# Kernel optimization log

Hardware: AMD Instinct MI355X
Metric: run time of the kernel (lower is better)

Reference implementation:

```python
import jax, jax.numpy as jnp
import numpy as np

H = 64      # h_dim
E = 64      # embedding_dim
L = 100     # latent_dim
T = 30      # seq_len
DT = 0.03

def _leaky(x):
    return jnp.where(x >= 0, x, 0.01 * x)  # nn.LeakyReLU default slope

def _mlp(h, Ws, bs, Wf, bf):
    # 3 stacked [H,H] LeakyReLU layers + final [L,H] layer, LeakyReLU after EVERY layer (as in source)
    for i in range(Ws.shape[0]):
        h = _leaky(h @ Ws[i].T + bs[i])
    return _leaky(h @ Wf.T + bf)

def _lstm_step(h, c, gates):
    # torch LSTM gate order: i, f, g, o
    i, f, g, o = jnp.split(gates, 4, axis=-1)
    c = jax.nn.sigmoid(f) * c + jax.nn.sigmoid(i) * jnp.tanh(g)
    h = jax.nn.sigmoid(o) * jnp.tanh(c)
    return h, c

def _forward(expert_traj, init_state, eps,
             W_se, b_se,
             W_ih_e, W_hh_e, b_ih_e, b_hh_e,
             mean_Ws, mean_bs, mean_Wf, mean_bf,
             lv_Ws, lv_bs, lv_Wf, lv_bf,
             W_init, b_init,
             W_ih_d, W_hh_d, b_ih_d, b_hh_d,
             W_c, b_c):
    B = expert_traj.shape[0]
    # --- encode: relative positions ---
    rel_xy = jnp.concatenate([expert_traj[:, :1, :2],
                              expert_traj[:, 1:, :2] - expert_traj[:, :-1, :2]], axis=1)
    inp = jnp.concatenate([rel_xy, expert_traj[:, :, 2:]], axis=-1)  # [B,T,4]
    emb = inp @ W_se.T + b_se                                        # [B,T,E]
    x_seq = jnp.swapaxes(emb, 0, 1)                                  # [T,B,E] seq-major
    # precompute input projection for all timesteps in one GEMM
    xp = x_seq @ W_ih_e.T + (b_ih_e + b_hh_e)                        # [T,B,4H]
    h0 = jnp.zeros((B, H), dtype=expert_traj.dtype)
    c0 = jnp.zeros((B, H), dtype=expert_traj.dtype)
    def enc_step(carry, xp_t):
        h, c = carry
        h, c = _lstm_step(h, c, xp_t + h @ W_hh_e.T)
        return (h, c), None
    (hT, _), _ = jax.lax.scan(enc_step, (h0, c0), xp)
    mu = _mlp(hT, mean_Ws, mean_bs, mean_Wf, mean_bf)                # [B,L]
    log_var = _mlp(hT, lv_Ws, lv_bs, lv_Wf, lv_bf)                   # [B,L]
    # --- reparameterize + tanh ---
    z = jnp.tanh(eps * jnp.exp(0.5 * log_var) + mu)
    # --- decode ---
    dh = z @ W_init.T + b_init                                       # [B,H], h0 = c0 = dh
    bias_d = b_ih_d + b_hh_d
    def dec_step(carry, _):
        h, c, prev = carry
        xe = prev @ W_se.T + b_se                                    # spatial embedding of state
        h, c = _lstm_step(h, c, xe @ W_ih_d.T + h @ W_hh_d.T + bias_d)
        ctrl = h @ W_c.T + b_c                                       # [B,2]
        pedal = ctrl[:, 0]
        steer = jnp.clip(ctrl[:, 1], -0.5, 0.5)
        x_t, y_t, psi, v = prev[:, 0], prev[:, 1], prev[:, 2], prev[:, 3]
        v1 = jnp.clip(v + pedal * DT, 0.0, 30.0)
        psi_dot = jnp.clip(v * jnp.tan(steer) / 2.5, -3.14 / 2, 3.14 / 2)
        cur = jnp.stack([x_t + v * jnp.cos(psi) * DT,
                         y_t + v * jnp.sin(psi) * DT,
                         psi + psi_dot * DT,
                         v1], axis=1)
        return (h, c, cur), cur
    _, traj = jax.lax.scan(dec_step, (dh, dh, init_state), None, length=T)
    recons = jnp.swapaxes(traj, 0, 1)                                # [B,T,4]
    return recons, expert_traj, mu, log_var

def setup_inputs() -> dict:
    key = jax.random.key(0)
    ks = jax.random.split(key, 32)
    B = 16384
    s = 0.05
    def p(k, shape):
        return jax.random.normal(k, shape, dtype=jnp.float32) * s
    return {
        "expert_traj": jax.random.normal(ks[0], (B, T, 4), dtype=jnp.float32),
        "init_state": jax.random.normal(ks[1], (B, 4), dtype=jnp.float32),
        "eps": jax.random.normal(ks[2], (B, L), dtype=jnp.float32),
        "W_se": p(ks[3], (E, 4)), "b_se": p(ks[4], (E,)),
        "W_ih_e": p(ks[5], (4 * H, E)), "W_hh_e": p(ks[6], (4 * H, H)),
        "b_ih_e": p(ks[7], (4 * H,)), "b_hh_e": p(ks[8], (4 * H,)),
        "mean_Ws": p(ks[9], (3, H, H)), "mean_bs": p(ks[10], (3, H)),
        "mean_Wf": p(ks[11], (L, H)), "mean_bf": p(ks[12], (L,)),
        "lv_Ws": p(ks[13], (3, H, H)), "lv_bs": p(ks[14], (3, H)),
        "lv_Wf": p(ks[15], (L, H)), "lv_bf": p(ks[16], (L,)),
        "W_init": p(ks[17], (H, L)), "b_init": p(ks[18], (H,)),
        "W_ih_d": p(ks[19], (4 * H, E)), "W_hh_d": p(ks[20], (4 * H, H)),
        "b_ih_d": p(ks[21], (4 * H,)), "b_hh_d": p(ks[22], (4 * H,)),
        "W_c": p(ks[23], (2, H)), "b_c": p(ks[24], (2,)),
    }

def reference(expert_traj, init_state, eps,
              W_se, b_se,
              W_ih_e, W_hh_e, b_ih_e, b_hh_e,
              mean_Ws, mean_bs, mean_Wf, mean_bf,
              lv_Ws, lv_bs, lv_Wf, lv_bf,
              W_init, b_init,
              W_ih_d, W_hh_d, b_ih_d, b_hh_d,
              W_c, b_c):
    return _forward(expert_traj, init_state, eps,
                    W_se, b_se,
                    W_ih_e, W_hh_e, b_ih_e, b_hh_e,
                    mean_Ws, mean_bs, mean_Wf, mean_bf,
                    lv_Ws, lv_bs, lv_Wf, lv_bf,
                    W_init, b_init,
                    W_ih_d, W_hh_d, b_ih_d, b_hh_d,
                    W_c, b_c)
```

## Files before the change

kernel.cpp:

```cpp
#include <hip/hip_runtime.h>

typedef unsigned short u16;
typedef unsigned int u32;
typedef __attribute__((ext_vector_type(8))) short bf16x8;
typedef __attribute__((ext_vector_type(4))) float f32x4;

#define B_TOT 16384
#define RPW 16
#define BLK 64
#define NBLK (B_TOT / RPW)
#define TT 30
#define LL 100
#define DTC 0.03f
#define L2E 1.44269504088896f

#define HST 104

#define OFF_HS  0
#define OFF_XS  3328
#define OFF_INP 5376
#define OFF_ZB  9216
#define SMEM_SZ 13568

#define WS_WHHE  0
#define WS_WHHD  18432
#define WS_MWS   36864
#define WS_LWS   49152
#define WS_MWF   61440
#define WS_LWF   67840
#define WS_WINIT 74240
#define WS_TOTAL 82432

__device__ __forceinline__ float bf2f(u16 u) {
    union { u32 i; float f; } v; v.i = ((u32)u) << 16; return v.f;
}
__device__ __forceinline__ u16 f2bf(float f) {
    union { float f; u32 i; } v; v.f = f;
    return (u16)((v.i + 0x7FFFu + ((v.i >> 16) & 1u)) >> 16);
}
__device__ __forceinline__ u16 f2bf_t(float f) {
    union { float f; u32 i; } v; v.f = f;
    return (u16)(v.i >> 16);
}
__device__ __forceinline__ float rcpf(float x) { return __builtin_amdgcn_rcpf(x); }
__device__ __forceinline__ float ex2(float x) { return __builtin_amdgcn_exp2f(x); }
__device__ __forceinline__ float tanh_(float x) {
    x = fminf(fmaxf(x, -15.f), 15.f);
    float e = __expf(2.f * x);
    return (e - 1.f) * rcpf(e + 1.f);
}
__device__ __forceinline__ float leaky(float x) { return x >= 0.f ? x : 0.01f * x; }
__device__ __forceinline__ f32x4 mfma16(bf16x8 a, bf16x8 b, f32x4 c) {
    return __builtin_amdgcn_mfma_f32_16x16x32_bf16(a, b, c, 0, 0, 0);
}

__global__ void setup_kernel(
    const float* __restrict__ W_se, const float* __restrict__ b_se,
    const float* __restrict__ W_ih_e, const float* __restrict__ W_hh_e,
    const float* __restrict__ b_ih_e, const float* __restrict__ b_hh_e,
    const float* __restrict__ W_ih_d, const float* __restrict__ W_hh_d,
    const float* __restrict__ b_ih_d, const float* __restrict__ b_hh_d,
    const float* __restrict__ mean_Ws, const float* __restrict__ lv_Ws,
    const float* __restrict__ mean_Wf, const float* __restrict__ lv_Wf,
    const float* __restrict__ W_init, u16* __restrict__ ws)
{
    const int gid = blockIdx.x * 256 + threadIdx.x;
    const int nth = gridDim.x * 256;
    for (int i = gid; i < 512; i += nth) {
        int which = i >> 8, row = i & 255, g = row >> 6;
        float s = (g == 2) ? 2.f * L2E : L2E;
        const float* wih = (which ? W_ih_d : W_ih_e) + row * 64;
        float f0=0,f1=0,f2=0,f3=0,fb=0;
        for (int e = 0; e < 64; ++e) {
            float w = wih[e];
            f0 = fmaf(w, W_se[e*4+0], f0);
            f1 = fmaf(w, W_se[e*4+1], f1);
            f2 = fmaf(w, W_se[e*4+2], f2);
            f3 = fmaf(w, W_se[e*4+3], f3);
            fb = fmaf(w, b_se[e], fb);
        }
        fb += (which ? b_ih_d : b_ih_e)[row] + (which ? b_hh_d : b_hh_e)[row];
        u16* dst = ws + (which ? WS_WHHD : WS_WHHE) + row * 72 + 64;
        dst[0]=f2bf(f0*s); dst[1]=f2bf(f1*s); dst[2]=f2bf(f2*s); dst[3]=f2bf(f3*s);
        dst[4]=f2bf(fb*s); dst[5]=0; dst[6]=0; dst[7]=0;
    }
    for (int i = gid; i < 2*16384; i += nth) {
        int which = i >= 16384;
        int j = which ? i - 16384 : i;
        int row = j >> 6, k = j & 63, g = row >> 6;
        float s = (g == 2) ? 2.f * L2E : L2E;
        const float* whh = which ? W_hh_d : W_hh_e;
        ws[(which ? WS_WHHD : WS_WHHE) + row*72 + k] = f2bf(whh[j] * s);
    }
    for (int i = gid; i < 12288; i += nth) {
        ws[WS_MWS + i] = f2bf(mean_Ws[i]);
        ws[WS_LWS + i] = f2bf(lv_Ws[i]);
    }
    for (int i = gid; i < 6400; i += nth) {
        ws[WS_MWF + i] = f2bf(mean_Wf[i]);
        ws[WS_LWF + i] = f2bf(lv_Wf[i]);
    }
    for (int i = gid; i < 8192; i += nth) {
        int r = i >> 7, k = i & 127;
        ws[WS_WINIT + i] = (k < LL) ? f2bf(W_init[r*LL + k]) : (u16)0;
    }
}

__global__ __launch_bounds__(BLK, 1) void vae_lstm_kernel(
    const float* __restrict__ expert, const float* __restrict__ init_state,
    const float* __restrict__ eps, const u16* __restrict__ ws,
    const float* __restrict__ mean_bs, const float* __restrict__ mean_bf,
    const float* __restrict__ lv_bs, const float* __restrict__ lv_bf,
    const float* __restrict__ b_init, const float* __restrict__ W_c,
    const float* __restrict__ b_c,
    float* __restrict__ out_recons, float* __restrict__ out_expert,
    float* __restrict__ out_mu, float* __restrict__ out_lv)
{
    const int l = threadIdx.x;
    const int lcol = l & 15;
    const int quad = l >> 4;
    const int b0 = blockIdx.x * RPW;

    __shared__ __align__(16) char smem[SMEM_SZ];
    u16* Hs  = (u16*)(smem + OFF_HS);
    u16* XS  = (u16*)(smem + OFF_XS);
    u16* inp = (u16*)(smem + OFF_INP);
    u16* zB  = (u16*)(smem + OFF_ZB);

    {
        u32* hz = (u32*)Hs;
#pragma unroll
        for (int i = 0; i < 13; ++i) hz[l + i * 64] = 0;
        if (l < RPW) Hs[l*HST + 68] = 0x3F80;
        u32* zz = (u32*)zB;
#pragma unroll
        for (int i = 0; i < 17; ++i) zz[l + i * 64] = 0;
        const int base = b0 * (TT*4);
#pragma unroll 4
        for (int i = 0; i < 30; ++i) {
            int idx = l + i * 64;
            int row = idx / 120, q = idx % 120;
            int t = q >> 2, k = q & 3;
            float v = expert[base + idx];
            out_expert[base + idx] = v;
            float r = v;
            if (k < 2 && t > 0) r = v - expert[base + idx - 4];
            u16 hv = f2bf(r);
            inp[row*120 + q] = hv;
            if (t == 0) Hs[row*HST + 64 + k] = hv;
        }
        __syncthreads();
    }

    float cst[4][4] = {};
    float hval[4][4];
    bf16x8 bw[4][4][3];

    auto build_bw = [&](const u16* wsW) {
#pragma unroll
        for (int g = 0; g < 4; ++g)
#pragma unroll
            for (int u = 0; u < 4; ++u) {
                const u16* wr = wsW + (g*64 + u*16 + lcol) * 72;
                bw[g][u][0] = *(const bf16x8*)(wr + quad*8);
                bw[g][u][1] = *(const bf16x8*)(wr + 32 + quad*8);
                if (quad == 0) {
                    bw[g][u][2] = *(const bf16x8*)(wr + 64);
                } else {
                    bf16x8 z;
#pragma unroll
                    for (int j = 0; j < 8; ++j) z[j] = 0;
                    bw[g][u][2] = z;
                }
            }
    };

    auto lstm_step = [&]() {
        const u16* hrow = Hs + lcol*HST;
        bf16x8 a0 = *(const bf16x8*)(hrow + quad*8);
        bf16x8 a1 = *(const bf16x8*)(hrow + 32 + quad*8);
        bf16x8 a2 = *(const bf16x8*)(hrow + 64 + quad*8);
        f32x4 acc[4][4];
#pragma unroll
        for (int g = 0; g < 4; ++g)
#pragma unroll
            for (int u = 0; u < 4; ++u) {
                f32x4 z = {0.f, 0.f, 0.f, 0.f};
                z = mfma16(a0, bw[g][u][0], z);
                z = mfma16(a1, bw[g][u][1], z);
                acc[g][u] = mfma16(a2, bw[g][u][2], z);
            }
#pragma unroll
        for (int u = 0; u < 4; ++u)
#pragma unroll
            for (int r = 0; r < 4; ++r) {
                float Ei = ex2(-acc[0][u][r]);
                float Ef = ex2(-acc[1][u][r]);
                float Eg = ex2(-acc[2][u][r]);
                float Eo = ex2(-acc[3][u][r]);
                float P = (1.f + Ei) * (1.f + Eg);
                float Q = 1.f + Ef;
                float num = fmaf(cst[u][r], P, (1.f - Eg) * Q);
                float cc = num * rcpf(P * Q);
                cst[u][r] = cc;
                float Ec = ex2(-2.f * L2E * cc);
                float h = (1.f - Ec) * rcpf((1.f + Eo) * (1.f + Ec));
                hval[u][r] = h;
                Hs[(quad*4 + r)*HST + u*16 + lcol] = f2bf_t(h);
            }
    };

    build_bw(ws + WS_WHHE);
    for (int stp = 0; stp < TT; ++stp) {
        lstm_step();
        if (stp < TT - 1) {
            int row = l >> 2, k = l & 3;
            Hs[row*HST + 64 + k] = inp[row*120 + (stp + 1)*4 + k];
        }
    }

    auto mlp_hidden = [&](bf16x8 a0, bf16x8 a1, const u16* wsW, const float* bg,
                          u16* outB, int ost) {
#pragma unroll
        for (int u = 0; u < 4; ++u) {
            int n = u*16 + lcol;
            const u16* wr = wsW + n*64;
            bf16x8 bb0 = *(const bf16x8*)(wr + quad*8);
            bf16x8 bb1 = *(const bf16x8*)(wr + 32 + quad*8);
            float bv = bg[n];
            f32x4 acc = {bv, bv, bv, bv};
            acc = mfma16(a0, bb0, acc);
            acc = mfma16(a1, bb1, acc);
#pragma unroll
            for (int r = 0; r < 4; ++r)
                outB[(quad*4 + r)*ost + n] = f2bf_t(leaky(acc[r]));
        }
    };

    {
        bf16x8 t0 = *(const bf16x8*)(Hs + lcol*HST + quad*8);
        bf16x8 t1 = *(const bf16x8*)(Hs + lcol*HST + 32 + quad*8);
        mlp_hidden(t0, t1, ws + WS_MWS, mean_bs, XS, 64);
        mlp_hidden(t0, t1, ws + WS_LWS, lv_bs, Hs, HST);
        bf16x8 m0 = *(const bf16x8*)(XS + lcol*64 + quad*8);
        bf16x8 m1 = *(const bf16x8*)(XS + lcol*64 + 32 + quad*8);
        mlp_hidden(m0, m1, ws + WS_MWS + 4096, mean_bs + 64, XS, 64);
        bf16x8 v0 = *(const bf16x8*)(Hs + lcol*HST + quad*8);
        bf16x8 v1 = *(const bf16x8*)(Hs + lcol*HST + 32 + quad*8);
        mlp_hidden(v0, v1, ws + WS_LWS + 4096, lv_bs + 64, Hs, HST);
        m0 = *(const bf16x8*)(XS + lcol*64 + quad*8);
        m1 = *(const bf16x8*)(XS + lcol*64 + 32 + quad*8);
        mlp_hidden(m0, m1, ws + WS_MWS + 8192, mean_bs + 128, XS, 64);
        v0 = *(const bf16x8*)(Hs + lcol*HST + quad*8);
        v1 = *(const bf16x8*)(Hs + lcol*HST + 32 + quad*8);
        mlp_hidden(v0, v1, ws + WS_LWS + 8192, lv_bs + 128, Hs, HST);
    }

    float muv[7][4];

    {
        bf16x8 fa = *(const bf16x8*)(XS + lcol*64 + quad*8);
        bf16x8 fb = *(const bf16x8*)(XS + lcol*64 + 32 + quad*8);
#pragma unroll
        for (int nt = 0; nt < 7; ++nt) {
            int n = nt*16 + lcol;
            bool ok = (n < LL);
            bf16x8 bb0, bb1;
            if (ok) {
                const u16* wr = ws + WS_MWF + n*64;
                bb0 = *(const bf16x8*)(wr + quad*8);
                bb1 = *(const bf16x8*)(wr + 32 + quad*8);
            } else {
#pragma unroll
                for (int j = 0; j < 8; ++j) { bb0[j] = 0; bb1[j] = 0; }
            }
            float bv = ok ? mean_bf[n] : 0.f;
            f32x4 acc = {bv, bv, bv, bv};
            acc = mfma16(fa, bb0, acc);
            acc = mfma16(fb, bb1, acc);
#pragma unroll
            for (int r = 0; r < 4; ++r) {
                float vv = leaky(acc[r]);
                muv[nt][r] = vv;
                if (ok) out_mu[(size_t)(b0 + quad*4 + r) * LL + n] = vv;
            }
        }
    }

    {
        bf16x8 fa = *(const bf16x8*)(Hs + lcol*HST + quad*8);
        bf16x8 fb = *(const bf16x8*)(Hs + lcol*HST + 32 + quad*8);
#pragma unroll
        for (int nt = 0; nt < 7; ++nt) {
            int n = nt*16 + lcol;
            bool ok = (n < LL);
            bf16x8 bb0, bb1;
            if (ok) {
                const u16* wr = ws + WS_LWF + n*64;
                bb0 = *(const bf16x8*)(wr + quad*8);
                bb1 = *(const bf16x8*)(wr + 32 + quad*8);
            } else {
#pragma unroll
                for (int j = 0; j < 8; ++j) { bb0[j] = 0; bb1[j] = 0; }
            }
            float bv = ok ? lv_bf[n] : 0.f;
            f32x4 acc = {bv, bv, bv, bv};
            acc = mfma16(fa, bb0, acc);
            acc = mfma16(fb, bb1, acc);
#pragma unroll
            for (int r = 0; r < 4; ++r) {
                if (ok) {
                    float lv = leaky(acc[r]);
                    size_t gi = (size_t)(b0 + quad*4 + r) * LL + n;
                    out_lv[gi] = lv;
                    float zv = tanh_(fmaf(eps[gi], __expf(0.5f * lv), muv[nt][r]));
                    zB[(quad*4 + r)*136 + n] = f2bf_t(zv);
                }
            }
        }
    }

    {
        bf16x8 az[4];
#pragma unroll
        for (int kt = 0; kt < 4; ++kt)
            az[kt] = *(const bf16x8*)(zB + lcol*136 + kt*32 + quad*8);
#pragma unroll
        for (int u = 0; u < 4; ++u) {
            int n = u*16 + lcol;
            float bv = b_init[n];
            f32x4 acc = {bv, bv, bv, bv};
#pragma unroll
            for (int kt = 0; kt < 4; ++kt) {
                bf16x8 bi = *(const bf16x8*)(ws + WS_WINIT + n*128 + kt*32 + quad*8);
                acc = mfma16(az[kt], bi, acc);
            }
#pragma unroll
            for (int r = 0; r < 4; ++r) {
                cst[u][r] = acc[r];
                Hs[(quad*4 + r)*HST + n] = f2bf_t(acc[r]);
            }
        }
    }

    {
        int row = l >> 2, k = l & 3;
        Hs[row*HST + 64 + k] = f2bf(init_state[(size_t)(b0 + row)*4 + k]);
    }
    float px = 0.f, py = 0.f, ppsi = 0.f, pv = 0.f;
    if (lcol < 4) {
        int row = quad*4 + lcol;
        const float* is = init_state + (size_t)(b0 + row)*4;
        px = is[0]; py = is[1]; ppsi = is[2]; pv = is[3];
    }
    float wc0[4], wc1[4];
#pragma unroll
    for (int u = 0; u < 4; ++u) {
        wc0[u] = W_c[u*16 + lcol];
        wc1[u] = W_c[64 + u*16 + lcol];
    }
    const float bc0 = b_c[0], bc1 = b_c[1];
    build_bw(ws + WS_WHHD);

    for (int stp = 0; stp < TT; ++stp) {
        lstm_step();
        float pa[4], pb[4];
#pragma unroll
        for (int r = 0; r < 4; ++r) {
            float s0 = 0.f, s1 = 0.f;
#pragma unroll
            for (int u = 0; u < 4; ++u) {
                s0 = fmaf(hval[u][r], wc0[u], s0);
                s1 = fmaf(hval[u][r], wc1[u], s1);
            }
            pa[r] = s0; pb[r] = s1;
        }
#pragma unroll
        for (int d = 1; d < 16; d <<= 1) {
#pragma unroll
            for (int r = 0; r < 4; ++r) {
                pa[r] += __shfl_xor(pa[r], d);
                pb[r] += __shfl_xor(pb[r], d);
            }
        }
        if (lcol < 4) {
            float a0s = lcol == 0 ? pa[0] : lcol == 1 ? pa[1] : lcol == 2 ? pa[2] : pa[3];
            float a1s = lcol == 0 ? pb[0] : lcol == 1 ? pb[1] : lcol == 2 ? pb[2] : pb[3];
            float pedal = a0s + bc0;
            float steer = fminf(fmaxf(a1s + bc1, -0.5f), 0.5f);
            float v1 = fminf(fmaxf(pv + pedal * DTC, 0.f), 30.f);
            float sn, cs;
            __sincosf(ppsi, &sn, &cs);
            float psid = fminf(fmaxf(pv * __tanf(steer) * 0.4f, -1.57f), 1.57f);
            float nx = fmaf(pv * cs, DTC, px);
            float ny = fmaf(pv * sn, DTC, py);
            float npsi = fmaf(psid, DTC, ppsi);
            px = nx; py = ny; ppsi = npsi; pv = v1;
            int row = quad*4 + lcol;
            float4 o; o.x = nx; o.y = ny; o.z = npsi; o.w = v1;
            *(float4*)(out_recons + ((size_t)(b0 + row) * TT + stp) * 4) = o;
            u32 lo = (u32)f2bf(nx) | ((u32)f2bf(ny) << 16);
            u32 hi = (u32)f2bf(npsi) | ((u32)f2bf(v1) << 16);
            uint2 pk; pk.x = lo; pk.y = hi;
            *(uint2*)(Hs + row*HST + 64) = pk;
        }
    }
}

extern "C" void kernel_launch(void* const* d_in, const int* in_sizes, int n_in,
                              void* d_out, int out_size, void* d_ws, size_t ws_size,
                              hipStream_t stream) {
    (void)in_sizes; (void)n_in; (void)ws_size; (void)out_size;
    const float* expert    = (const float*)d_in[0];
    const float* init_st   = (const float*)d_in[1];
    const float* eps       = (const float*)d_in[2];
    const float* W_se      = (const float*)d_in[3];
    const float* b_se      = (const float*)d_in[4];
    const float* W_ih_e    = (const float*)d_in[5];
    const float* W_hh_e    = (const float*)d_in[6];
    const float* b_ih_e    = (const float*)d_in[7];
    const float* b_hh_e    = (const float*)d_in[8];
    const float* mean_Ws   = (const float*)d_in[9];
    const float* mean_bs   = (const float*)d_in[10];
    const float* mean_Wf   = (const float*)d_in[11];
    const float* mean_bf   = (const float*)d_in[12];
    const float* lv_Ws     = (const float*)d_in[13];
    const float* lv_bs     = (const float*)d_in[14];
    const float* lv_Wf     = (const float*)d_in[15];
    const float* lv_bf     = (const float*)d_in[16];
    const float* W_init    = (const float*)d_in[17];
    const float* b_init    = (const float*)d_in[18];
    const float* W_ih_d    = (const float*)d_in[19];
    const float* W_hh_d    = (const float*)d_in[20];
    const float* b_ih_d    = (const float*)d_in[21];
    const float* b_hh_d    = (const float*)d_in[22];
    const float* W_c       = (const float*)d_in[23];
    const float* b_c       = (const float*)d_in[24];

    float* out = (float*)d_out;
    const size_t n_traj = (size_t)B_TOT * TT * 4;
    const size_t n_lat  = (size_t)B_TOT * LL;
    float* out_recons = out;
    float* out_expert = out + n_traj;
    float* out_mu     = out + 2 * n_traj;
    float* out_lv     = out + 2 * n_traj + n_lat;

    u16* ws = (u16*)d_ws;

    setup_kernel<<<64, 256, 0, stream>>>(
        W_se, b_se, W_ih_e, W_hh_e, b_ih_e, b_hh_e,
        W_ih_d, W_hh_d, b_ih_d, b_hh_d,
        mean_Ws, lv_Ws, mean_Wf, lv_Wf, W_init, ws);

    vae_lstm_kernel<<<NBLK, BLK, 0, stream>>>(
        expert, init_st, eps, ws,
        mean_bs, mean_bf, lv_bs, lv_bf, b_init, W_c, b_c,
        out_recons, out_expert, out_mu, out_lv);
}
```

Measured before the change: 250.2 us.

## Split LSTM hidden units across two waves with double-buffered shared state

```diff
diff --git a/kernel.cpp b/kernel.cpp
--- a/kernel.cpp
+++ b/kernel.cpp
@@ -6,21 +6,22 @@
 typedef __attribute__((ext_vector_type(4))) float f32x4;
 
 #define B_TOT 16384
-#define RPW 16
-#define BLK 64
-#define NBLK (B_TOT / RPW)
+#define RR 16
+#define BLK 128
+#define NBLK (B_TOT / RR)
 #define TT 30
 #define LL 100
 #define DTC 0.03f
 #define L2E 1.44269504088896f
 
 #define HST 104
-
-#define OFF_HS  0
-#define OFF_XS  3328
-#define OFF_INP 5376
-#define OFF_ZB  9216
-#define SMEM_SZ 13568
+#define HBUF (RR * HST)
+
+#define OFF_H   0
+#define OFF_XS  6656
+#define OFF_INP 10752
+#define OFF_ZB  14592
+#define SMEM_SZ 18944
 
 #define WS_WHHE  0
 #define WS_WHHD  18432
@@ -106,7 +107,7 @@
     }
 }
 
-__global__ __launch_bounds__(BLK, 1) void vae_lstm_kernel(
+__global__ __launch_bounds__(BLK, 2) void vae_lstm_kernel(
     const float* __restrict__ expert, const float* __restrict__ init_state,
     const float* __restrict__ eps, const u16* __restrict__ ws,
     const float* __restrict__ mean_bs, const float* __restrict__ mean_bf,
@@ -116,29 +117,32 @@
     float* __restrict__ out_recons, float* __restrict__ out_expert,
     float* __restrict__ out_mu, float* __restrict__ out_lv)
 {
-    const int l = threadIdx.x;
+    const int tid = threadIdx.x;
+    const int wv = tid >> 6;
+    const int l = tid & 63;
     const int lcol = l & 15;
     const int quad = l >> 4;
-    const int b0 = blockIdx.x * RPW;
+    const int ubase = wv * 32;
+    const int b0 = blockIdx.x * RR;
 
     __shared__ __align__(16) char smem[SMEM_SZ];
-    u16* Hs  = (u16*)(smem + OFF_HS);
+    u16* Hb  = (u16*)(smem + OFF_H);
     u16* XS  = (u16*)(smem + OFF_XS);
+    u16* XA  = XS;
+    u16* XB  = XS + RR*64;
     u16* inp = (u16*)(smem + OFF_INP);
     u16* zB  = (u16*)(smem + OFF_ZB);
+    float* sc = (float*)XS;
 
     {
-        u32* hz = (u32*)Hs;
-#pragma unroll
-        for (int i = 0; i < 13; ++i) hz[l + i * 64] = 0;
-        if (l < RPW) Hs[l*HST + 68] = 0x3F80;
+        u32* hz = (u32*)Hb;
+        for (int idx = tid; idx < 2*RR*52; idx += BLK) hz[idx] = 0;
         u32* zz = (u32*)zB;
-#pragma unroll
-        for (int i = 0; i < 17; ++i) zz[l + i * 64] = 0;
+        for (int idx = tid; idx < RR*68; idx += BLK) zz[idx] = 0;
+        __syncthreads();
+        if (tid < 32) Hb[(tid >> 4)*HBUF + (tid & 15)*HST + 68] = 0x3F80;
         const int base = b0 * (TT*4);
-#pragma unroll 4
-        for (int i = 0; i < 30; ++i) {
-            int idx = l + i * 64;
+        for (int idx = tid; idx < RR*TT*4; idx += BLK) {
             int row = idx / 120, q = idx % 120;
             int t = q >> 2, k = q & 3;
             float v = expert[base + idx];
@@ -147,83 +151,90 @@
             if (k < 2 && t > 0) r = v - expert[base + idx - 4];
             u16 hv = f2bf(r);
             inp[row*120 + q] = hv;
-            if (t == 0) Hs[row*HST + 64 + k] = hv;
-        }
-        __syncthreads();
-    }
-
-    float cst[4][4] = {};
-    float hval[4][4];
-    bf16x8 bw[4][4][3];
+            if (t == 0) Hb[row*HST + 64 + k] = hv;
+        }
+        __syncthreads();
+    }
+
+    float cst[2][4] = {};
+    float hval[2][4];
+    bf16x8 bw[4][2][3];
 
     auto build_bw = [&](const u16* wsW) {
 #pragma unroll
         for (int g = 0; g < 4; ++g)
 #pragma unroll
-            for (int u = 0; u < 4; ++u) {
-                const u16* wr = wsW + (g*64 + u*16 + lcol) * 72;
-                bw[g][u][0] = *(const bf16x8*)(wr + quad*8);
-                bw[g][u][1] = *(const bf16x8*)(wr + 32 + quad*8);
+            for (int ul = 0; ul < 2; ++ul) {
+                const u16* wr = wsW + (g*64 + ubase + ul*16 + lcol) * 72;
+                bw[g][ul][0] = *(const bf16x8*)(wr + quad*8);
+                bw[g][ul][1] = *(const bf16x8*)(wr + 32 + quad*8);
                 if (quad == 0) {
-                    bw[g][u][2] = *(const bf16x8*)(wr + 64);
+                    bw[g][ul][2] = *(const bf16x8*)(wr + 64);
                 } else {
                     bf16x8 z;
 #pragma unroll
                     for (int j = 0; j < 8; ++j) z[j] = 0;
-                    bw[g][u][2] = z;
+                    bw[g][ul][2] = z;
                 }
             }
     };
 
-    auto lstm_step = [&]() {
-        const u16* hrow = Hs + lcol*HST;
+    auto lstm_step = [&](const u16* Hc, u16* Hn) {
+        const u16* hrow = Hc + lcol*HST;
         bf16x8 a0 = *(const bf16x8*)(hrow + quad*8);
         bf16x8 a1 = *(const bf16x8*)(hrow + 32 + quad*8);
         bf16x8 a2 = *(const bf16x8*)(hrow + 64 + quad*8);
-        f32x4 acc[4][4];
+        f32x4 acc[4][2];
 #pragma unroll
         for (int g = 0; g < 4; ++g)
 #pragma unroll
-            for (int u = 0; u < 4; ++u) {
+            for (int ul = 0; ul < 2; ++ul) {
                 f32x4 z = {0.f, 0.f, 0.f, 0.f};
-                z = mfma16(a0, bw[g][u][0], z);
-                z = mfma16(a1, bw[g][u][1], z);
-                acc[g][u] = mfma16(a2, bw[g][u][2], z);
-            }
-#pragma unroll
-        for (int u = 0; u < 4; ++u)
-#pragma unroll
-            for (int r = 0; r < 4; ++r) {
-                float Ei = ex2(-acc[0][u][r]);
-                float Ef = ex2(-acc[1][u][r]);
-                float Eg = ex2(-acc[2][u][r]);
-                float Eo = ex2(-acc[3][u][r]);
+                z = mfma16(a0, bw[g][ul][0], z);
+                z = mfma16(a1, bw[g][ul][1], z);
+                acc[g][ul] = mfma16(a2, bw[g][ul][2], z);
+            }
+#pragma unroll
+        for (int ul = 0; ul < 2; ++ul)
+#pragma unroll
+            for (int r = 0; r < 4; ++r) {
+                float Ei = ex2(-acc[0][ul][r]);
+                float Ef = ex2(-acc[1][ul][r]);
+                float Eg = ex2(-acc[2][ul][r]);
+                float Eo = ex2(-acc[3][ul][r]);
                 float P = (1.f + Ei) * (1.f + Eg);
                 float Q = 1.f + Ef;
-                float num = fmaf(cst[u][r], P, (1.f - Eg) * Q);
+                float num = fmaf(cst[ul][r], P, (1.f - Eg) * Q);
                 float cc = num * rcpf(P * Q);
-                cst[u][r] = cc;
+                cst[ul][r] = cc;
                 float Ec = ex2(-2.f * L2E * cc);
                 float h = (1.f - Ec) * rcpf((1.f + Eo) * (1.f + Ec));
-                hval[u][r] = h;
-                Hs[(quad*4 + r)*HST + u*16 + lcol] = f2bf_t(h);
+                hval[ul][r] = h;
+                Hn[(quad*4 + r)*HST + ubase + ul*16 + lcol] = f2bf_t(h);
             }
     };
 
     build_bw(ws + WS_WHHE);
     for (int stp = 0; stp < TT; ++stp) {
-        lstm_step();
-        if (stp < TT - 1) {
+        const u16* Hc = Hb + (stp & 1) * HBUF;
+        u16* Hn = Hb + ((stp + 1) & 1) * HBUF;
+        lstm_step(Hc, Hn);
+        if (wv == 0 && stp < TT - 1) {
             int row = l >> 2, k = l & 3;
-            Hs[row*HST + 64 + k] = inp[row*120 + (stp + 1)*4 + k];
-        }
-    }
-
-    auto mlp_hidden = [&](bf16x8 a0, bf16x8 a1, const u16* wsW, const float* bg,
-                          u16* outB, int ost) {
-#pragma unroll
-        for (int u = 0; u < 4; ++u) {
-            int n = u*16 + lcol;
+            Hn[row*HST + 64 + k] = inp[row*120 + (stp + 1)*4 + k];
+        }
+        __syncthreads();
+    }
+    u16* H0 = Hb;
+    u16* H1 = Hb + HBUF;
+
+    auto mlp_hidden = [&](const u16* inB, int ist, u16* outB, int ost,
+                          const u16* wsW, const float* bg) {
+        bf16x8 a0 = *(const bf16x8*)(inB + lcol*ist + quad*8);
+        bf16x8 a1 = *(const bf16x8*)(inB + lcol*ist + 32 + quad*8);
+#pragma unroll
+        for (int ul = 0; ul < 2; ++ul) {
+            int n = ubase + ul*16 + lcol;
             const u16* wr = wsW + n*64;
             bf16x8 bb0 = *(const bf16x8*)(wr + quad*8);
             bf16x8 bb1 = *(const bf16x8*)(wr + 32 + quad*8);
@@ -235,34 +246,22 @@
             for (int r = 0; r < 4; ++r)
                 outB[(quad*4 + r)*ost + n] = f2bf_t(leaky(acc[r]));
         }
+        __syncthreads();
     };
 
+    mlp_hidden(H0, HST, XA, 64, ws + WS_MWS,        mean_bs);
+    mlp_hidden(XA, 64,  XB, 64, ws + WS_MWS + 4096, mean_bs + 64);
+    mlp_hidden(XB, 64,  XA, 64, ws + WS_MWS + 8192, mean_bs + 128);
+
+    float muv[4][4];
+
     {
-        bf16x8 t0 = *(const bf16x8*)(Hs + lcol*HST + quad*8);
-        bf16x8 t1 = *(const bf16x8*)(Hs + lcol*HST + 32 + quad*8);
-        mlp_hidden(t0, t1, ws + WS_MWS, mean_bs, XS, 64);
-        mlp_hidden(t0, t1, ws + WS_LWS, lv_bs, Hs, HST);
-        bf16x8 m0 = *(const bf16x8*)(XS + lcol*64 + quad*8);
-        bf16x8 m1 = *(const bf16x8*)(XS + lcol*64 + 32 + quad*8);
-        mlp_hidden(m0, m1, ws + WS_MWS + 4096, mean_bs + 64, XS, 64);
-        bf16x8 v0 = *(const bf16x8*)(Hs + lcol*HST + quad*8);
-        bf16x8 v1 = *(const bf16x8*)(Hs + lcol*HST + 32 + quad*8);
-        mlp_hidden(v0, v1, ws + WS_LWS + 4096, lv_bs + 64, Hs, HST);
-        m0 = *(const bf16x8*)(XS + lcol*64 + quad*8);
-        m1 = *(const bf16x8*)(XS + lcol*64 + 32 + quad*8);
-        mlp_hidden(m0, m1, ws + WS_MWS + 8192, mean_bs + 128, XS, 64);
-        v0 = *(const bf16x8*)(Hs + lcol*HST + quad*8);
-        v1 = *(const bf16x8*)(Hs + lcol*HST + 32 + quad*8);
-        mlp_hidden(v0, v1, ws + WS_LWS + 8192, lv_bs + 128, Hs, HST);
-    }
-
-    float muv[7][4];
-
-    {
-        bf16x8 fa = *(const bf16x8*)(XS + lcol*64 + quad*8);
-        bf16x8 fb = *(const bf16x8*)(XS + lcol*64 + 32 + quad*8);
-#pragma unroll
-        for (int nt = 0; nt < 7; ++nt) {
+        bf16x8 fa = *(const bf16x8*)(XA + lcol*64 + quad*8);
+        bf16x8 fb = *(const bf16x8*)(XA + lcol*64 + 32 + quad*8);
+#pragma unroll
+        for (int ti = 0; ti < 4; ++ti) {
+            int nt = wv + ti*2;
+            if (nt > 6) continue;
             int n = nt*16 + lcol;
             bool ok = (n < LL);
             bf16x8 bb0, bb1;
@@ -281,17 +280,23 @@
 #pragma unroll
             for (int r = 0; r < 4; ++r) {
                 float vv = leaky(acc[r]);
-                muv[nt][r] = vv;
+                muv[ti][r] = vv;
                 if (ok) out_mu[(size_t)(b0 + quad*4 + r) * LL + n] = vv;
             }
         }
     }
 
+    mlp_hidden(H0, HST, H1, HST, ws + WS_LWS,        lv_bs);
+    mlp_hidden(H1, HST, H0, HST, ws + WS_LWS + 4096, lv_bs + 64);
+    mlp_hidden(H0, HST, H1, HST, ws + WS_LWS + 8192, lv_bs + 128);
+
     {
-        bf16x8 fa = *(const bf16x8*)(Hs + lcol*HST + quad*8);
-        bf16x8 fb = *(const bf16x8*)(Hs + lcol*HST + 32 + quad*8);
-#pragma unroll
-        for (int nt = 0; nt < 7; ++nt) {
+        bf16x8 fa = *(const bf16x8*)(H1 + lcol*HST + quad*8);
+        bf16x8 fb = *(const bf16x8*)(H1 + lcol*HST + 32 + quad*8);
+#pragma unroll
+        for (int ti = 0; ti < 4; ++ti) {
+            int nt = wv + ti*2;
+            if (nt > 6) continue;
             int n = nt*16 + lcol;
             bool ok = (n < LL);
             bf16x8 bb0, bb1;
@@ -313,11 +318,12 @@
                     float lv = leaky(acc[r]);
                     size_t gi = (size_t)(b0 + quad*4 + r) * LL + n;
                     out_lv[gi] = lv;
-                    float zv = tanh_(fmaf(eps[gi], __expf(0.5f * lv), muv[nt][r]));
+                    float zv = tanh_(fmaf(eps[gi], __expf(0.5f * lv), muv[ti][r]));
                     zB[(quad*4 + r)*136 + n] = f2bf_t(zv);
                 }
             }
         }
+        __syncthreads();
     }
 
     {
@@ -326,8 +332,8 @@
         for (int kt = 0; kt < 4; ++kt)
             az[kt] = *(const bf16x8*)(zB + lcol*136 + kt*32 + quad*8);
 #pragma unroll
-        for (int u = 0; u < 4; ++u) {
-            int n = u*16 + lcol;
+        for (int ul = 0; ul < 2; ++ul) {
+            int n = ubase + ul*16 + lcol;
             float bv = b_init[n];
             f32x4 acc = {bv, bv, bv, bv};
 #pragma unroll
@@ -337,43 +343,40 @@
             }
 #pragma unroll
             for (int r = 0; r < 4; ++r) {
-                cst[u][r] = acc[r];
-                Hs[(quad*4 + r)*HST + n] = f2bf_t(acc[r]);
-            }
-        }
-    }
-
-    {
+                cst[ul][r] = acc[r];
+                H0[(quad*4 + r)*HST + n] = f2bf_t(acc[r]);
+            }
+        }
+    }
+
+    if (wv == 0) {
         int row = l >> 2, k = l & 3;
-        Hs[row*HST + 64 + k] = f2bf(init_state[(size_t)(b0 + row)*4 + k]);
+        H0[row*HST + 64 + k] = f2bf(init_state[(size_t)(b0 + row)*4 + k]);
     }
     float px = 0.f, py = 0.f, ppsi = 0.f, pv = 0.f;
-    if (lcol < 4) {
-        int row = quad*4 + lcol;
-        const float* is = init_state + (size_t)(b0 + row)*4;
+    if (tid < 16) {
+        const float* is = init_state + (size_t)(b0 + tid)*4;
         px = is[0]; py = is[1]; ppsi = is[2]; pv = is[3];
     }
-    float wc0[4], wc1[4];
-#pragma unroll
-    for (int u = 0; u < 4; ++u) {
-        wc0[u] = W_c[u*16 + lcol];
-        wc1[u] = W_c[64 + u*16 + lcol];
+    float wc0[2], wc1[2];
+#pragma unroll
+    for (int ul = 0; ul < 2; ++ul) {
+        wc0[ul] = W_c[ubase + ul*16 + lcol];
+        wc1[ul] = W_c[64 + ubase + ul*16 + lcol];
     }
     const float bc0 = b_c[0], bc1 = b_c[1];
     build_bw(ws + WS_WHHD);
+    __syncthreads();
 
     for (int stp = 0; stp < TT; ++stp) {
-        lstm_step();
+        const u16* Hc = Hb + (stp & 1) * HBUF;
+        u16* Hn = Hb + ((stp + 1) & 1) * HBUF;
+        lstm_step(Hc, Hn);
         float pa[4], pb[4];
 #pragma unroll
         for (int r = 0; r < 4; ++r) {
-            float s0 = 0.f, s1 = 0.f;
-#pragma unroll
-            for (int u = 0; u < 4; ++u) {
-                s0 = fmaf(hval[u][r], wc0[u], s0);
-                s1 = fmaf(hval[u][r], wc1[u], s1);
-            }
-            pa[r] = s0; pb[r] = s1;
+            pa[r] = fmaf(hval[0][r], wc0[0], hval[1][r] * wc0[1]);
+            pb[r] = fmaf(hval[0][r], wc1[0], hval[1][r] * wc1[1]);
         }
 #pragma unroll
         for (int d = 1; d < 16; d <<= 1) {
@@ -383,11 +386,18 @@
                 pb[r] += __shfl_xor(pb[r], d);
             }
         }
-        if (lcol < 4) {
-            float a0s = lcol == 0 ? pa[0] : lcol == 1 ? pa[1] : lcol == 2 ? pa[2] : pa[3];
-            float a1s = lcol == 0 ? pb[0] : lcol == 1 ? pb[1] : lcol == 2 ? pb[2] : pb[3];
-            float pedal = a0s + bc0;
-            float steer = fminf(fmaxf(a1s + bc1, -0.5f), 0.5f);
+        if (lcol == 0) {
+#pragma unroll
+            for (int r = 0; r < 4; ++r) {
+                sc[wv*32 + quad*4 + r]      = pa[r];
+                sc[wv*32 + 16 + quad*4 + r] = pb[r];
+            }
+        }
+        __syncthreads();
+        if (tid < 16) {
+            int row = tid;
+            float pedal = sc[row] + sc[32 + row] + bc0;
+            float steer = fminf(fmaxf(sc[16 + row] + sc[48 + row] + bc1, -0.5f), 0.5f);
             float v1 = fminf(fmaxf(pv + pedal * DTC, 0.f), 30.f);
             float sn, cs;
             __sincosf(ppsi, &sn, &cs);
@@ -396,14 +406,14 @@
             float ny = fmaf(pv * sn, DTC, py);
             float npsi = fmaf(psid, DTC, ppsi);
             px = nx; py = ny; ppsi = npsi; pv = v1;
-            int row = quad*4 + lcol;
             float4 o; o.x = nx; o.y = ny; o.z = npsi; o.w = v1;
             *(float4*)(out_recons + ((size_t)(b0 + row) * TT + stp) * 4) = o;
             u32 lo = (u32)f2bf(nx) | ((u32)f2bf(ny) << 16);
             u32 hi = (u32)f2bf(npsi) | ((u32)f2bf(v1) << 16);
             uint2 pk; pk.x = lo; pk.y = hi;
-            *(uint2*)(Hs + row*HST + 64) = pk;
-        }
+            *(uint2*)(Hn + row*HST + 64) = pk;
+        }
+        __syncthreads();
     }
 }
 
```

Result: faster. 227.9 us (-8.9%).

## Transpose LSTM MFMA so hidden state stays in registers via ds_bpermute

Applied to the files above, without the earlier changes.

```diff
diff --git a/kernel.cpp b/kernel.cpp
--- a/kernel.cpp
+++ b/kernel.cpp
@@ -41,6 +41,12 @@
 __device__ __forceinline__ u16 f2bf_t(float f) {
     union { float f; u32 i; } v; v.f = f;
     return (u16)(v.i >> 16);
+}
+__device__ __forceinline__ u32 pkt(float a, float b) {
+    return (u32)f2bf_t(a) | ((u32)f2bf_t(b) << 16);
+}
+__device__ __forceinline__ u32 pkr(float a, float b) {
+    return (u32)f2bf(a) | ((u32)f2bf(b) << 16);
 }
 __device__ __forceinline__ float rcpf(float x) { return __builtin_amdgcn_rcpf(x); }
 __device__ __forceinline__ float ex2(float x) { return __builtin_amdgcn_exp2f(x); }
@@ -117,7 +123,7 @@
     float* __restrict__ out_mu, float* __restrict__ out_lv)
 {
     const int l = threadIdx.x;
-    const int lcol = l & 15;
+    const int lc = l & 15;
     const int quad = l >> 4;
     const int b0 = blockIdx.x * RPW;
 
@@ -126,12 +132,9 @@
     u16* XS  = (u16*)(smem + OFF_XS);
     u16* inp = (u16*)(smem + OFF_INP);
     u16* zB  = (u16*)(smem + OFF_ZB);
+    float* dhS = (float*)(smem + OFF_ZB);
 
     {
-        u32* hz = (u32*)Hs;
-#pragma unroll
-        for (int i = 0; i < 13; ++i) hz[l + i * 64] = 0;
-        if (l < RPW) Hs[l*HST + 68] = 0x3F80;
         u32* zz = (u32*)zB;
 #pragma unroll
         for (int i = 0; i < 17; ++i) zz[l + i * 64] = 0;
@@ -145,85 +148,104 @@
             out_expert[base + idx] = v;
             float r = v;
             if (k < 2 && t > 0) r = v - expert[base + idx - 4];
-            u16 hv = f2bf(r);
-            inp[row*120 + q] = hv;
-            if (t == 0) Hs[row*HST + 64 + k] = hv;
+            inp[row*120 + q] = f2bf(r);
         }
         __syncthreads();
     }
 
+    bf16x8 AW[4][4][3];
+    auto loadW = [&](const u16* wsW) {
+#pragma unroll
+        for (int g = 0; g < 4; ++g)
+#pragma unroll
+            for (int ub = 0; ub < 4; ++ub)
+#pragma unroll
+                for (int kb = 0; kb < 3; ++kb)
+                    AW[g][ub][kb] = *(const bf16x8*)(wsW + (g*64 + ub*16 + lc)*72
+                                                    + kb*32 + quad*8);
+    };
+
+    u32 P[4][2] = {{0,0},{0,0},{0,0},{0,0}};
     float cst[4][4] = {};
     float hval[4][4];
-    bf16x8 bw[4][4][3];
-
-    auto build_bw = [&](const u16* wsW) {
+    const int aLo = ((quad & 1)*32 + lc) * 4;
+    const int aHi = aLo + 64;
+
+    auto bsel = [&](u32 plo, u32 phi, int addr) -> u32 {
+        int t0 = __builtin_amdgcn_ds_bpermute(addr, (int)plo);
+        int t1 = __builtin_amdgcn_ds_bpermute(addr, (int)phi);
+        return (u32)(quad < 2 ? t0 : t1);
+    };
+
+    union U8 { bf16x8 v; u32 w[4]; };
+
+    auto lstm_step = [&](u32 b2w0, u32 b2w1) {
+        U8 B0, B1, B2;
+        B0.w[0] = bsel(P[0][0], P[1][0], aLo);
+        B0.w[1] = bsel(P[0][1], P[1][1], aLo);
+        B0.w[2] = bsel(P[0][0], P[1][0], aHi);
+        B0.w[3] = bsel(P[0][1], P[1][1], aHi);
+        B1.w[0] = bsel(P[2][0], P[3][0], aLo);
+        B1.w[1] = bsel(P[2][1], P[3][1], aLo);
+        B1.w[2] = bsel(P[2][0], P[3][0], aHi);
+        B1.w[3] = bsel(P[2][1], P[3][1], aHi);
+        B2.w[0] = b2w0; B2.w[1] = b2w1;
+        B2.w[2] = (quad == 0) ? 0x00003F80u : 0u;
+        B2.w[3] = 0u;
+        f32x4 acc[4][4];
 #pragma unroll
         for (int g = 0; g < 4; ++g)
 #pragma unroll
-            for (int u = 0; u < 4; ++u) {
-                const u16* wr = wsW + (g*64 + u*16 + lcol) * 72;
-                bw[g][u][0] = *(const bf16x8*)(wr + quad*8);
-                bw[g][u][1] = *(const bf16x8*)(wr + 32 + quad*8);
-                if (quad == 0) {
-                    bw[g][u][2] = *(const bf16x8*)(wr + 64);
-                } else {
-                    bf16x8 z;
-#pragma unroll
-                    for (int j = 0; j < 8; ++j) z[j] = 0;
-                    bw[g][u][2] = z;
-                }
-            }
+            for (int ub = 0; ub < 4; ++ub) {
+                f32x4 z = {0.f, 0.f, 0.f, 0.f};
+                z = mfma16(AW[g][ub][0], B0.v, z);
+                z = mfma16(AW[g][ub][1], B1.v, z);
+                acc[g][ub] = mfma16(AW[g][ub][2], B2.v, z);
+            }
+#pragma unroll
+        for (int ub = 0; ub < 4; ++ub) {
+#pragma unroll
+            for (int r = 0; r < 4; ++r) {
+                float Ei = ex2(-acc[0][ub][r]);
+                float Ef = ex2(-acc[1][ub][r]);
+                float Eg = ex2(-acc[2][ub][r]);
+                float Eo = ex2(-acc[3][ub][r]);
+                float Pp = (1.f + Ei) * (1.f + Eg);
+                float Qq = 1.f + Ef;
+                float num = fmaf(cst[ub][r], Pp, (1.f - Eg) * Qq);
+                float cc = num * rcpf(Pp * Qq);
+                cst[ub][r] = cc;
+                float Ec = ex2(-2.f * L2E * cc);
+                hval[ub][r] = (1.f - Ec) * rcpf((1.f + Eo) * (1.f + Ec));
+            }
+            P[ub][0] = pkt(hval[ub][0], hval[ub][1]);
+            P[ub][1] = pkt(hval[ub][2], hval[ub][3]);
+        }
     };
 
-    auto lstm_step = [&]() {
-        const u16* hrow = Hs + lcol*HST;
-        bf16x8 a0 = *(const bf16x8*)(hrow + quad*8);
-        bf16x8 a1 = *(const bf16x8*)(hrow + 32 + quad*8);
-        bf16x8 a2 = *(const bf16x8*)(hrow + 64 + quad*8);
-        f32x4 acc[4][4];
-#pragma unroll
-        for (int g = 0; g < 4; ++g)
-#pragma unroll
-            for (int u = 0; u < 4; ++u) {
-                f32x4 z = {0.f, 0.f, 0.f, 0.f};
-                z = mfma16(a0, bw[g][u][0], z);
-                z = mfma16(a1, bw[g][u][1], z);
-                acc[g][u] = mfma16(a2, bw[g][u][2], z);
-            }
-#pragma unroll
-        for (int u = 0; u < 4; ++u)
-#pragma unroll
-            for (int r = 0; r < 4; ++r) {
-                float Ei = ex2(-acc[0][u][r]);
-                float Ef = ex2(-acc[1][u][r]);
-                float Eg = ex2(-acc[2][u][r]);
-                float Eo = ex2(-acc[3][u][r]);
-                float P = (1.f + Ei) * (1.f + Eg);
-                float Q = 1.f + Ef;
-                float num = fmaf(cst[u][r], P, (1.f - Eg) * Q);
-                float cc = num * rcpf(P * Q);
-                cst[u][r] = cc;
-                float Ec = ex2(-2.f * L2E * cc);
-                float h = (1.f - Ec) * rcpf((1.f + Eo) * (1.f + Ec));
-                hval[u][r] = h;
-                Hs[(quad*4 + r)*HST + u*16 + lcol] = f2bf_t(h);
-            }
-    };
-
-    build_bw(ws + WS_WHHE);
+    loadW(ws + WS_WHHE);
     for (int stp = 0; stp < TT; ++stp) {
-        lstm_step();
-        if (stp < TT - 1) {
-            int row = l >> 2, k = l & 3;
-            Hs[row*HST + 64 + k] = inp[row*120 + (stp + 1)*4 + k];
-        }
-    }
+        u32 x0 = 0, x1 = 0;
+        if (l < 16) {
+            const u16* xp = inp + l*120 + stp*4;
+            x0 = *(const u32*)xp;
+            x1 = *(const u32*)(xp + 2);
+        }
+        lstm_step(x0, x1);
+    }
+
+#pragma unroll
+    for (int ub = 0; ub < 4; ++ub) {
+        *(u32*)(Hs + lc*HST + ub*16 + quad*4)     = P[ub][0];
+        *(u32*)(Hs + lc*HST + ub*16 + quad*4 + 2) = P[ub][1];
+    }
+    __syncthreads();
 
     auto mlp_hidden = [&](bf16x8 a0, bf16x8 a1, const u16* wsW, const float* bg,
                           u16* outB, int ost) {
 #pragma unroll
         for (int u = 0; u < 4; ++u) {
-            int n = u*16 + lcol;
+            int n = u*16 + lc;
             const u16* wr = wsW + n*64;
             bf16x8 bb0 = *(const bf16x8*)(wr + quad*8);
             bf16x8 bb1 = *(const bf16x8*)(wr + 32 + quad*8);
@@ -238,32 +260,32 @@
     };
 
     {
-        bf16x8 t0 = *(const bf16x8*)(Hs + lcol*HST + quad*8);
-        bf16x8 t1 = *(const bf16x8*)(Hs + lcol*HST + 32 + quad*8);
+        bf16x8 t0 = *(const bf16x8*)(Hs + lc*HST + quad*8);
+        bf16x8 t1 = *(const bf16x8*)(Hs + lc*HST + 32 + quad*8);
         mlp_hidden(t0, t1, ws + WS_MWS, mean_bs, XS, 64);
         mlp_hidden(t0, t1, ws + WS_LWS, lv_bs, Hs, HST);
-        bf16x8 m0 = *(const bf16x8*)(XS + lcol*64 + quad*8);
-        bf16x8 m1 = *(const bf16x8*)(XS + lcol*64 + 32 + quad*8);
+        bf16x8 m0 = *(const bf16x8*)(XS + lc*64 + quad*8);
+        bf16x8 m1 = *(const bf16x8*)(XS + lc*64 + 32 + quad*8);
         mlp_hidden(m0, m1, ws + WS_MWS + 4096, mean_bs + 64, XS, 64);
-        bf16x8 v0 = *(const bf16x8*)(Hs + lcol*HST + quad*8);
-        bf16x8 v1 = *(const bf16x8*)(Hs + lcol*HST + 32 + quad*8);
+        bf16x8 v0 = *(const bf16x8*)(Hs + lc*HST + quad*8);
+        bf16x8 v1 = *(const bf16x8*)(Hs + lc*HST + 32 + quad*8);
         mlp_hidden(v0, v1, ws + WS_LWS + 4096, lv_bs + 64, Hs, HST);
-        m0 = *(const bf16x8*)(XS + lcol*64 + quad*8);
-        m1 = *(const bf16x8*)(XS + lcol*64 + 32 + quad*8);
+        m0 = *(const bf16x8*)(XS + lc*64 + quad*8);
+        m1 = *(const bf16x8*)(XS + lc*64 + 32 + quad*8);
         mlp_hidden(m0, m1, ws + WS_MWS + 8192, mean_bs + 128, XS, 64);
-        v0 = *(const bf16x8*)(Hs + lcol*HST + quad*8);
-        v1 = *(const bf16x8*)(Hs + lcol*HST + 32 + quad*8);
+        v0 = *(const bf16x8*)(Hs + lc*HST + quad*8);
+        v1 = *(const bf16x8*)(Hs + lc*HST + 32 + quad*8);
         mlp_hidden(v0, v1, ws + WS_LWS + 8192, lv_bs + 128, Hs, HST);
     }
 
     float muv[7][4];
 
     {
-        bf16x8 fa = *(const bf16x8*)(XS + lcol*64 + quad*8);
-        bf16x8 fb = *(const bf16x8*)(XS + lcol*64 + 32 + quad*8);
+        bf16x8 fa = *(const bf16x8*)(XS + lc*64 + quad*8);
+        bf16x8 fb = *(const bf16x8*)(XS + lc*64 + 32 + quad*8);
 #pragma unroll
         for (int nt = 0; nt < 7; ++nt) {
-            int n = nt*16 + lcol;
+            int n = nt*16 + lc;
             bool ok = (n < LL);
             bf16x8 bb0, bb1;
             if (ok) {
@@ -288,11 +310,11 @@
     }
 
     {
-        bf16x8 fa = *(const bf16x8*)(Hs + lcol*HST + quad*8);
-        bf16x8 fb = *(const bf16x8*)(Hs + lcol*HST + 32 + quad*8);
+        bf16x8 fa = *(const bf16x8*)(Hs + lc*HST + quad*8);
+        bf16x8 fb = *(const bf16x8*)(Hs + lc*HST + 32 + quad*8);
 #pragma unroll
         for (int nt = 0; nt < 7; ++nt) {
-            int n = nt*16 + lcol;
+            int n = nt*16 + lc;
             bool ok = (n < LL);
             bf16x8 bb0, bb1;
             if (ok) {
@@ -324,10 +346,10 @@
         bf16x8 az[4];
 #pragma unroll
         for (int kt = 0; kt < 4; ++kt)
-            az[kt] = *(const bf16x8*)(zB + lcol*136 + kt*32 + quad*8);
+            az[kt] = *(const bf16x8*)(zB + lc*136 + kt*32 + quad*8);
 #pragma unroll
         for (int u = 0; u < 4; ++u) {
-            int n = u*16 + lcol;
+            int n = u*16 + lc;
             float bv = b_init[n];
             f32x4 acc = {bv, bv, bv, bv};
 #pragma unroll
@@ -336,58 +358,55 @@
                 acc = mfma16(az[kt], bi, acc);
             }
 #pragma unroll
+            for (int r = 0; r < 4; ++r)
+                dhS[(quad*4 + r)*64 + n] = acc[r];
+        }
+    }
+
+#pragma unroll
+    for (int ub = 0; ub < 4; ++ub) {
+        f32x4 d4 = *(const f32x4*)(dhS + lc*64 + ub*16 + quad*4);
+#pragma unroll
+        for (int r = 0; r < 4; ++r) cst[ub][r] = d4[r];
+        P[ub][0] = pkt(d4[0], d4[1]);
+        P[ub][1] = pkt(d4[2], d4[3]);
+    }
+
+    loadW(ws + WS_WHHD);
+    float wcp[4][4], wcs[4][4];
+#pragma unroll
+    for (int ub = 0; ub < 4; ++ub)
+#pragma unroll
+        for (int r = 0; r < 4; ++r) {
+            int u = ub*16 + quad*4 + r;
+            wcp[ub][r] = W_c[u];
+            wcs[ub][r] = W_c[64 + u];
+        }
+    const float bc0 = b_c[0], bc1 = b_c[1];
+    float px = 0.f, py = 0.f, ppsi = 0.f, pv = 0.f;
+    u32 xw0 = 0, xw1 = 0;
+    if (l < 16) {
+        const float* is = init_state + (size_t)(b0 + l)*4;
+        px = is[0]; py = is[1]; ppsi = is[2]; pv = is[3];
+        xw0 = pkr(px, py);
+        xw1 = pkr(ppsi, pv);
+    }
+
+    for (int stp = 0; stp < TT; ++stp) {
+        lstm_step(xw0, xw1);
+        float p0 = 0.f, p1 = 0.f;
+#pragma unroll
+        for (int ub = 0; ub < 4; ++ub)
+#pragma unroll
             for (int r = 0; r < 4; ++r) {
-                cst[u][r] = acc[r];
-                Hs[(quad*4 + r)*HST + n] = f2bf_t(acc[r]);
-            }
-        }
-    }
-
-    {
-        int row = l >> 2, k = l & 3;
-        Hs[row*HST + 64 + k] = f2bf(init_state[(size_t)(b0 + row)*4 + k]);
-    }
-    float px = 0.f, py = 0.f, ppsi = 0.f, pv = 0.f;
-    if (lcol < 4) {
-        int row = quad*4 + lcol;
-        const float* is = init_state + (size_t)(b0 + row)*4;
-        px = is[0]; py = is[1]; ppsi = is[2]; pv = is[3];
-    }
-    float wc0[4], wc1[4];
-#pragma unroll
-    for (int u = 0; u < 4; ++u) {
-        wc0[u] = W_c[u*16 + lcol];
-        wc1[u] = W_c[64 + u*16 + lcol];
-    }
-    const float bc0 = b_c[0], bc1 = b_c[1];
-    build_bw(ws + WS_WHHD);
-
-    for (int stp = 0; stp < TT; ++stp) {
-        lstm_step();
-        float pa[4], pb[4];
-#pragma unroll
-        for (int r = 0; r < 4; ++r) {
-            float s0 = 0.f, s1 = 0.f;
-#pragma unroll
-            for (int u = 0; u < 4; ++u) {
-                s0 = fmaf(hval[u][r], wc0[u], s0);
-                s1 = fmaf(hval[u][r], wc1[u], s1);
-            }
-            pa[r] = s0; pb[r] = s1;
-        }
-#pragma unroll
-        for (int d = 1; d < 16; d <<= 1) {
-#pragma unroll
-            for (int r = 0; r < 4; ++r) {
-                pa[r] += __shfl_xor(pa[r], d);
-                pb[r] += __shfl_xor(pb[r], d);
-            }
-        }
-        if (lcol < 4) {
-            float a0s = lcol == 0 ? pa[0] : lcol == 1 ? pa[1] : lcol == 2 ? pa[2] : pa[3];
-            float a1s = lcol == 0 ? pb[0] : lcol == 1 ? pb[1] : lcol == 2 ? pb[2] : pb[3];
-            float pedal = a0s + bc0;
-            float steer = fminf(fmaxf(a1s + bc1, -0.5f), 0.5f);
+                p0 = fmaf(hval[ub][r], wcp[ub][r], p0);
+                p1 = fmaf(hval[ub][r], wcs[ub][r], p1);
+            }
+        p0 += __shfl_xor(p0, 16); p1 += __shfl_xor(p1, 16);
+        p0 += __shfl_xor(p0, 32); p1 += __shfl_xor(p1, 32);
+        if (l < 16) {
+            float pedal = p0 + bc0;
+            float steer = fminf(fmaxf(p1 + bc1, -0.5f), 0.5f);
             float v1 = fminf(fmaxf(pv + pedal * DTC, 0.f), 30.f);
             float sn, cs;
             __sincosf(ppsi, &sn, &cs);
@@ -396,13 +415,10 @@
             float ny = fmaf(pv * sn, DTC, py);
             float npsi = fmaf(psid, DTC, ppsi);
             px = nx; py = ny; ppsi = npsi; pv = v1;
-            int row = quad*4 + lcol;
             float4 o; o.x = nx; o.y = ny; o.z = npsi; o.w = v1;
-            *(float4*)(out_recons + ((size_t)(b0 + row) * TT + stp) * 4) = o;
-            u32 lo = (u32)f2bf(nx) | ((u32)f2bf(ny) << 16);
-            u32 hi = (u32)f2bf(npsi) | ((u32)f2bf(v1) << 16);
-            uint2 pk; pk.x = lo; pk.y = hi;
-            *(uint2*)(Hs + row*HST + 64) = pk;
+            *(float4*)(out_recons + ((size_t)(b0 + l) * TT + stp) * 4) = o;
+            xw0 = pkr(nx, ny);
+            xw1 = pkr(npsi, v1);
         }
     }
 }
```

New measurement: 239.9 us. -4.1%, faster.
